# Performance work log

Measured on AMD Instinct MI355X. Metric: run time of the kernel, lower is better.

The kernel has to match this reference:

```python
import jax, jax.numpy as jnp
import numpy as np

B, N, MODES, WIDTH = 4, 8192, 12, 32
TWO = 2 * MODES  # 24
M_TOT = TWO * (TWO - 1)  # 552


def setup_inputs() -> dict:
    key = jax.random.key(0)
    ks = jax.random.split(key, 12)
    scale = 1.0 / (WIDTH * WIDTH)
    x = jax.random.uniform(ks[0], (B, N, 2), jnp.float32)
    fc0_w = jax.random.normal(ks[1], (2, WIDTH), jnp.float32) * 0.1
    fc0_b = jax.random.normal(ks[2], (WIDTH,), jnp.float32) * 0.05
    # 4 layers x {weights1, weights2}, stored as real/imag pairs (torch.rand cfloat ~ U[0,1)+1j*U[0,1))
    spec_w = jax.random.uniform(ks[3], (4, 2, WIDTH, WIDTH, MODES, MODES, 2), jnp.float32) * scale
    conv_w = jax.random.normal(ks[4], (4, WIDTH, WIDTH), jnp.float32) * 0.1  # Conv1d k=1 -> [O,I]
    conv_b = jax.random.normal(ks[5], (4, WIDTH), jnp.float32) * 0.05
    fc1_w = jax.random.normal(ks[6], (WIDTH, 128), jnp.float32) * 0.1
    fc1_b = jax.random.normal(ks[7], (128,), jnp.float32) * 0.05
    fc2_w = jax.random.normal(ks[8], (128, 1), jnp.float32) * 0.1
    fc2_b = jax.random.normal(ks[9], (1,), jnp.float32) * 0.05
    return {"x": x, "fc0_w": fc0_w, "fc0_b": fc0_b, "spec_w": spec_w,
            "conv_w": conv_w, "conv_b": conv_b, "fc1_w": fc1_w, "fc1_b": fc1_b,
            "fc2_w": fc2_w, "fc2_b": fc2_b}


def _vft_matrices(xp, yp):
    # xp, yp: [B, N], already min-shifted and scaled to [0, 6.28]
    kx = jnp.concatenate([jnp.arange(MODES), jnp.arange(-MODES, 0)]).astype(jnp.float32)       # [24]
    ky = jnp.concatenate([jnp.arange(MODES), jnp.arange(-(MODES - 1), 0)]).astype(jnp.float32)  # [23]
    Xm = kx[None, :, None] * xp[:, None, :]  # [B,24,N]
    Ym = ky[None, :, None] * yp[:, None, :]  # [B,23,N]
    # torch: X repeat(1,23,1) tiles blocks; Y repeat(1,1,24).reshape interleaves -> row j*24+i = X[i]+Y[j]
    phase = jnp.tile(Xm, (1, TWO - 1, 1)) + jnp.repeat(Ym, TWO, axis=1)  # [B,552,N]
    V_fwd = jnp.exp(-1j * phase)                    # [B,552,N] complex64
    V_inv = jnp.conj(V_fwd).transpose(0, 2, 1)      # [B,N,552]
    return V_fwd, V_inv


def _spectral_conv(h, V_fwd, V_inv, w1, w2):
    # h: [B,C,N] real; w1,w2: [C,C,M,M] complex
    b, c, n = h.shape
    # forward Vandermonde transform: bmm(V_fwd, h^T) then permute -> [B,C,552]
    x_ft = jnp.einsum('bmn,bnc->bcm', V_fwd, h.astype(jnp.complex64).transpose(0, 2, 1))
    x_ft = x_ft.reshape(b, c, TWO, TWO - 1)
    top = jnp.einsum('bixy,ioxy->boxy', x_ft[:, :, :MODES, :MODES], w1)
    bot = jnp.einsum('bixy,ioxy->boxy', x_ft[:, :, -MODES:, :MODES], w2)
    out_ft = jnp.zeros((b, WIDTH, TWO, MODES), jnp.complex64)
    out_ft = out_ft.at[:, :, :MODES, :MODES].set(top)
    out_ft = out_ft.at[:, :, -MODES:, :MODES].set(bot)
    x_ft = out_ft.reshape(b, WIDTH, 2 * MODES * MODES)  # [B,C,288]
    # conjugate-symmetric completion (flip over last two dims, as in source)
    x_ft2 = jnp.conj(jnp.flip(x_ft[..., TWO:], axis=(-2, -1)))  # [B,C,264]
    x_ft = jnp.concatenate([x_ft, x_ft2], axis=-1)  # [B,C,552]
    out = jnp.einsum('bnm,bmc->bcn', V_inv, x_ft.transpose(0, 2, 1))  # [B,C,N]
    return (out / n * 2).real


def reference(x, fc0_w, fc0_b, spec_w, conv_w, conv_b, fc1_w, fc1_b, fc2_w, fc2_b):
    gelu = lambda t: jax.nn.gelu(t, approximate=False)
    # VFT mutates x in-place by subtracting global mins (view semantics in torch)
    xp = x[:, :, 0] - jnp.min(x[:, :, 0])
    yp = x[:, :, 1] - jnp.min(x[:, :, 1])
    x_in = jnp.stack([xp, yp], axis=-1)  # what fc0 actually sees
    V_fwd, V_inv = _vft_matrices(xp * 6.28 / jnp.max(xp), yp * 6.28 / jnp.max(yp))
    h = (x_in @ fc0_w + fc0_b).transpose(0, 2, 1)  # [B,C,N]
    for l in range(4):
        w1 = spec_w[l, 0, ..., 0] + 1j * spec_w[l, 0, ..., 1]
        w2 = spec_w[l, 1, ..., 0] + 1j * spec_w[l, 1, ..., 1]
        x1 = _spectral_conv(h, V_fwd, V_inv, w1, w2)
        x2 = jnp.einsum('bin,oi->bon', h, conv_w[l]) + conv_b[l][None, :, None]
        h = x1 + x2
        if l < 3:
            h = gelu(h)
    h = h.transpose(0, 2, 1)  # [B,N,C]
    h = gelu(h @ fc1_w + fc1_b)
    return h @ fc2_w + fc2_b  # [B,N,1]
```

## Files before the change

### kernel.cpp

```cpp
#include <hip/hip_runtime.h>
#include <cmath>

#define NB 4
#define NN 8192
#define CH 32

typedef short short8 __attribute__((ext_vector_type(8)));
typedef float floatx4 __attribute__((ext_vector_type(4)));
typedef unsigned short ushort_t;

__device__ __forceinline__ unsigned short f2b(float f){
  unsigned u = __float_as_uint(f);
  u = u + 0x7FFFu + ((u >> 16) & 1u);
  return (unsigned short)(u >> 16);
}
__device__ __forceinline__ float b2f(unsigned short h){
  return __uint_as_float(((unsigned)h) << 16);
}
__device__ __forceinline__ float gelu_f(float v){
  return 0.5f * v * (1.0f + erff(v * 0.70710678118654752440f));
}
__device__ __forceinline__ int repk(int t){
  int j = t / 24, i = t - j * 24;
  if(j == 0)  return (i <= 12) ? i : -1;
  if(j <= 11) return 13 + (j - 1) * 24 + i;
  return (i == 12) ? 277 + (j - 12) : -1;
}
__device__ __forceinline__ int partner(int t){
  int j = t / 24, i = t - j * 24;
  return ((23 - j) % 23) * 24 + ((24 - i) % 24);
}
__device__ __forceinline__ int repT(int k){
  if(k < 13) return k;
  if(k < 277){ int m = k - 13; return (m / 24 + 1) * 24 + (m % 24); }
  return (k - 277 + 12) * 24 + 12;
}

__global__ __launch_bounds__(256) void k_pre(const float* __restrict__ spec,
    float2* __restrict__ wt, const float* __restrict__ x, float4* __restrict__ pmm,
    const float* __restrict__ fc1w, ushort_t* __restrict__ WB,
    const float* __restrict__ convw, ushort_t* __restrict__ WA)
{
  const int tid = threadIdx.x;
  if(blockIdx.x < 128){
    int g = blockIdx.x * 256 + tid;
    float a = x[(size_t)g * 2], b = x[(size_t)g * 2 + 1];
    float mn0 = a, mx0 = a, mn1 = b, mx1 = b;
    for(int off = 32; off > 0; off >>= 1){
      mn0 = fminf(mn0, __shfl_down(mn0, off));
      mx0 = fmaxf(mx0, __shfl_down(mx0, off));
      mn1 = fminf(mn1, __shfl_down(mn1, off));
      mx1 = fmaxf(mx1, __shfl_down(mx1, off));
    }
    __shared__ float4 wp[4];
    if((tid & 63) == 0) wp[tid >> 6] = make_float4(mn0, mn1, mx0, mx1);
    __syncthreads();
    if(tid == 0){
      float4 r = wp[0];
      for(int i2 = 1; i2 < 4; ++i2){
        float4 v = wp[i2];
        r.x = fminf(r.x, v.x); r.y = fminf(r.y, v.y);
        r.z = fmaxf(r.z, v.z); r.w = fmaxf(r.w, v.w);
      }
      pmm[blockIdx.x] = r;
    }
  } else if(blockIdx.x < 4736){
    int g = (blockIdx.x - 128) * 256 + tid;
    int o  = g & 31;
    int i  = (g >> 5) & 31;
    int rest = g >> 10;
    int pq = rest % 144;
    int ls = rest / 144;
    wt[g] = ((const float2*)spec)[(((size_t)(ls * 32 + i) * 32 + o) * 144 + pq)];
  } else {
    for(int s = tid; s < 512; s += 256){
      int jt = s >> 6, l = s & 63;
      int c = l & 15, qq = l >> 4;
      #pragma unroll
      for(int e = 0; e < 8; ++e){
        float wv = fc1w[(qq * 8 + e) * 128 + jt * 16 + c];
        ushort_t hi = f2b(wv);
        WB[(jt * 64 + l) * 8 + e] = hi;
        WB[4096 + (jt * 64 + l) * 8 + e] = f2b(wv - b2f(hi));
      }
    }
    for(int s = tid; s < 8192; s += 256){
      int l2   = s >> 11;
      int rem  = s & 2047;
      int limb = rem >> 10;
      int rem2 = rem & 1023;
      int half = rem2 >> 9;
      int le   = rem2 & 511;
      int lane = le >> 3, e = le & 7;
      int c = half * 16 + (lane & 15);
      int i = (lane >> 4) * 8 + e;
      float wv = convw[((size_t)l2 * 32 + c) * 32 + i] * 4096.0f;
      ushort_t hi = f2b(wv);
      WA[s] = limb ? f2b(wv - b2f(hi)) : hi;
    }
  }
}

__global__ __launch_bounds__(256) void k_vbuild(const float* __restrict__ x,
    const float4* __restrict__ pmm, const float* __restrict__ fw,
    const float* __restrict__ fb, ushort_t* __restrict__ AF, ushort_t* __restrict__ VTF,
    ushort_t* __restrict__ hbB, ushort_t* __restrict__ hbChi, ushort_t* __restrict__ hbClo)
{
  __shared__ ushort_t lds1[32 * 584];
  __shared__ float4 mmv;
  const int tid = threadIdx.x;
  if(tid < 64){
    float4 a = pmm[tid], c = pmm[tid + 64];
    float mn0 = fminf(a.x, c.x), mn1 = fminf(a.y, c.y);
    float mx0 = fmaxf(a.z, c.z), mx1 = fmaxf(a.w, c.w);
    for(int off = 32; off > 0; off >>= 1){
      mn0 = fminf(mn0, __shfl_down(mn0, off));
      mn1 = fminf(mn1, __shfl_down(mn1, off));
      mx0 = fmaxf(mx0, __shfl_down(mx0, off));
      mx1 = fmaxf(mx1, __shfl_down(mx1, off));
    }
    if(tid == 0) mmv = make_float4(mn0, mn1, mx0, mx1);
  }
  __syncthreads();
  const int nl = tid & 31, part = tid >> 5;
  const int b = blockIdx.x >> 8;
  const int nblk = blockIdx.x & 255;
  const int n = nblk * 32 + nl;
  float mn0 = mmv.x, mn1 = mmv.y, mx0 = mmv.z, mx1 = mmv.w;
  float x0 = x[(size_t)(b * NN + n) * 2]     - mn0;
  float x1 = x[(size_t)(b * NN + n) * 2 + 1] - mn1;
  float sp = x0 * (6.28f / (mx0 - mn0));
  float sq = x1 * (6.28f / (mx1 - mn1));
  float cx, sx, cy, sy;
  sincosf(sp, &sx, &cx);
  sincosf(sq, &sy, &cy);
  int j0 = part * 3;
  int j1 = (j0 + 3 < 23) ? j0 + 3 : 23;
  float ky0 = (j0 < 12) ? (float)j0 : (float)(j0 - 23);
  float cb, sb;
  sincosf(ky0 * sq, &sb, &cb);
  for(int j = j0; j < j1; ++j){
    float ca = 1.0f, sa = 0.0f;
    #pragma unroll
    for(int i = 0; i < 24; ++i){
      float vr = ca * cb - sa * sb;
      float vi = -(sa * cb + ca * sb);
      int t = j * 24 + i;
      int k = repk(t);
      if(k >= 0){
        lds1[nl * 584 + k]       = f2b(vr);
        lds1[nl * 584 + 288 + k] = f2b(vi);
      }
      float cn = ca * cx - sa * sx;
      float sn = sa * cx + ca * sx;
      if(i == 11) sn = -sn;
      ca = cn; sa = sn;
    }
    float cbn = cb * cy - sb * sy;
    float sbn = sb * cy + cb * sy;
    cb = cbn; sb = sbn;
  }
  __syncthreads();
  #pragma unroll
  for(int r = 0; r < 9; ++r){
    int c = tid + 256 * r;
    int t16 = c / 1152;
    int c2 = c - t16 * 1152;
    int kk = c2 >> 6;
    int rem = c2 & 63;
    int q = rem >> 4, n15 = rem & 15;
    short8 v = *(const short8*)(lds1 + (t16 * 16 + n15) * 584 + kk * 32 + q * 8);
    *(short8*)(VTF + ((size_t)((b * 512 + nblk * 2 + t16) * 18 + kk)) * 512
               + (q * 16 + n15) * 8) = v;
  }
  #pragma unroll
  for(int r = 0; r < 9; ++r){
    int c = tid + 256 * r;
    int st = c >> 6;
    int rem = c & 63;
    int q = rem >> 4, srow = rem & 15;
    int sg = st * 16 + srow;
    int s = (sg < 288) ? sg : sg - 288;
    int sinh_ = (sg >= 288);
    int p2 = s / 12, qq = s - p2 * 12;
    int t = p2 * 23 + qq;
    int k = repk(t);
    unsigned short flip = 0;
    if(k < 0){ k = repk(partner(t)); if(sinh_) flip = 0x8000; }
    int col = sinh_ ? 288 + k : k;
    ushort_t tmp[8];
    #pragma unroll
    for(int e = 0; e < 8; ++e)
      tmp[e] = lds1[(q * 8 + e) * 584 + col] ^ flip;
    *(short8*)(AF + ((size_t)((b * 36 + st) * 256 + nblk)) * 512
               + (q * 16 + srow) * 8) = *(short8*)tmp;
  }
  #pragma unroll
  for(int rr = 0; rr < 4; ++rr){
    int c2 = part + rr * 8;
    float v = fb[c2] + x0 * fw[c2] + x1 * fw[32 + c2];
    ushort_t hi = f2b(v), lo = f2b(v - b2f(hi));
    int half = c2 >> 4, cl = c2 & 15;
    hbB[(((size_t)(b * 2 + half) * 256 + nblk) * 512) + ((nl >> 3) * 16 + cl) * 8 + (nl & 7)] = hi;
    size_t ca = ((size_t)(b * 512 + nblk * 2 + (nl >> 4))) * 512
              + ((c2 >> 3) * 16 + (nl & 15)) * 8 + (c2 & 7);
    hbChi[ca] = hi; hbClo[ca] = lo;
  }
}

__global__ __launch_bounds__(256) void k_fwd(const ushort_t* __restrict__ AF,
    const ushort_t* __restrict__ hbB, float* __restrict__ xp)
{
  const int stp = blockIdx.x;
  const int ks = blockIdx.y;
  const int b  = blockIdx.z;
  const int w = threadIdx.x >> 6;
  const int lane = threadIdx.x & 63;
  const int row = lane & 15;
  const int q = lane >> 4;
  const int st0 = stp * 2;
  const size_t abase0 = ((size_t)(b * 36 + st0) * 256) * 512 + (q * 16 + row) * 8;
  const size_t abase1 = abase0 + (size_t)256 * 512;
  const size_t hB0 = ((size_t)(b * 2 + 0) * 256) * 512 + (size_t)lane * 8;
  const size_t hB1 = ((size_t)(b * 2 + 1) * 256) * 512 + (size_t)lane * 8;
  floatx4 aA0 = {0.f,0.f,0.f,0.f}, aA1 = {0.f,0.f,0.f,0.f};
  floatx4 aB0 = {0.f,0.f,0.f,0.f}, aB1 = {0.f,0.f,0.f,0.f};
  #pragma unroll
  for(int kk = 0; kk < 4; ++kk){
    int g = ks * 16 + w * 4 + kk;
    short8 A0 = *(const short8*)(AF + abase0 + (size_t)g * 512);
    short8 A1 = *(const short8*)(AF + abase1 + (size_t)g * 512);
    short8 B0 = *(const short8*)(hbB + hB0 + (size_t)g * 512);
    short8 B1 = *(const short8*)(hbB + hB1 + (size_t)g * 512);
    aA0 = __builtin_amdgcn_mfma_f32_16x16x32_bf16(A0, B0, aA0, 0, 0, 0);
    aA1 = __builtin_amdgcn_mfma_f32_16x16x32_bf16(A0, B1, aA1, 0, 0, 0);
    aB0 = __builtin_amdgcn_mfma_f32_16x16x32_bf16(A1, B0, aB0, 0, 0, 0);
    aB1 = __builtin_amdgcn_mfma_f32_16x16x32_bf16(A1, B1, aB1, 0, 0, 0);
  }
  __shared__ float red[4 * 512];
  const int e = threadIdx.x;
  const int eo = e & 31;
  #pragma unroll
  for(int r = 0; r < 4; ++r){
    int rrow = q * 4 + r;
    red[w * 512 + rrow * 32 + row]      = aA0[r];
    red[w * 512 + rrow * 32 + 16 + row] = aA1[r];
  }
  __syncthreads();
  {
    float v0 = red[e] + red[512 + e] + red[1024 + e] + red[1536 + e];
    float v1 = red[e + 256] + red[512 + e + 256] + red[1024 + e + 256] + red[1536 + e + 256];
    size_t r0 = (size_t)(b * 576 + st0 * 16 + (e >> 5));
    xp[(r0 * 16 + ks) * 32 + eo]       = v0;
    xp[((r0 + 8) * 16 + ks) * 32 + eo] = v1;
  }
  __syncthreads();
  #pragma unroll
  for(int r = 0; r < 4; ++r){
    int rrow = q * 4 + r;
    red[w * 512 + rrow * 32 + row]      = aB0[r];
    red[w * 512 + rrow * 32 + 16 + row] = aB1[r];
  }
  __syncthreads();
  {
    float v0 = red[e] + red[512 + e] + red[1024 + e] + red[1536 + e];
    float v1 = red[e + 256] + red[512 + e + 256] + red[1024 + e + 256] + red[1536 + e + 256];
    size_t r0 = (size_t)(b * 576 + (st0 + 1) * 16 + (e >> 5));
    xp[(r0 * 16 + ks) * 32 + eo]       = v0;
    xp[((r0 + 8) * 16 + ks) * 32 + eo] = v1;
  }
}

__global__ __launch_bounds__(256) void k_mixg(const float* __restrict__ xp,
    const float2* __restrict__ wt, ushort_t* __restrict__ ghi, ushort_t* __restrict__ glof,
    int layer)
{
  const int wv = threadIdx.x >> 6;
  const int lane = threadIdx.x & 63;
  const int k = blockIdx.x;
  const int b = blockIdx.y;
  const int t = repT(k);
  const int j = t / 24, i = t - j * 24;
  const int u = partner(t);
  const bool unpaired = (i == 12) || (u == t);
  const int idxT = (t < 288) ? t : 575 - t;  const bool cfT = (t >= 288);
  const int idxU = (u < 288) ? u : 575 - u;  const bool cfU = (u >= 288);
  __shared__ float Xs[2][64];
  __shared__ float FrP[2][2][32], FiP[2][2][32];
  {
    const int m = wv & 1, hf = wv >> 1;
    int idx = m ? idxU : idxT;
    int rrow = hf ? 288 + idx : idx;
    const float* sb = xp + (size_t)(b * 576 + rrow) * 512;
    float4 a = *(const float4*)(sb + lane * 4);
    float4 c = *(const float4*)(sb + 256 + lane * 4);
    a.x += c.x; a.y += c.y; a.z += c.z; a.w += c.w;
    #pragma unroll
    for(int mk = 8; mk <= 32; mk <<= 1){
      a.x += __shfl_xor(a.x, mk);
      a.y += __shfl_xor(a.y, mk);
      a.z += __shfl_xor(a.z, mk);
      a.w += __shfl_xor(a.w, mk);
    }
    if(lane < 8){
      int o0 = hf * 32 + lane * 4;
      Xs[m][o0 + 0] = a.x;
      Xs[m][o0 + 1] = a.y;
      Xs[m][o0 + 2] = a.z;
      Xs[m][o0 + 3] = a.w;
    }
  }
  __syncthreads();
  {
    const int m = wv & 1, ih = wv >> 1;
    int idx = m ? idxU : idxT;
    int p2 = idx / 12, qq = idx - p2 * 12;
    int sel = (p2 < 12) ? 0 : 1;
    int pq = (p2 % 12) * 12 + qq;
    const float2* wb = wt + ((size_t)((layer * 2 + sel) * 144 + pq)) * 1024;
    if(lane < 32){
      const int o = lane;
      float fr = 0.f, fi = 0.f;
      #pragma unroll
      for(int ii = 0; ii < 16; ++ii){
        int i2 = ih * 16 + ii;
        float xr = Xs[m][i2], xi = Xs[m][32 + i2];
        float2 wvv = wb[i2 * 32 + o];
        fr += xr * wvv.x - xi * wvv.y;
        fi += xr * wvv.y + xi * wvv.x;
      }
      FrP[m][ih][o] = fr; FiP[m][ih][o] = fi;
    }
  }
  __syncthreads();
  if(wv == 0 && lane < 32){
    const int c = lane;
    const int srcT = cfT ? 31 - c : c;
    const int srcU = cfU ? 31 - c : c;
    float fax = FrP[0][0][srcT] + FrP[0][1][srcT];
    float fay = FiP[0][0][srcT] + FiP[0][1][srcT];
    float fbx = FrP[1][0][srcU] + FrP[1][1][srcU];
    float fby = FiP[1][0][srcU] + FiP[1][1][srcU];
    float gr = fax;
    float gi = cfT ? -fay : fay;
    if(!unpaired){
      gr += fbx;
      gi -= (cfU ? -fby : fby);
    }
    unsigned short hr = f2b(gr); float lr = gr - b2f(hr);
    unsigned short hi2 = f2b(gi); float li = gi - b2f(hi2);
    size_t base = (size_t)(b * CH + c) * 576;
    ghi[base + k] = hr;          ghi[base + 288 + k] = hi2;
    int hhc = c >> 4, cl = c & 15;
    int kk1 = k >> 5, q1 = (k >> 3) & 3, e1 = k & 7;
    size_t fb2 = (size_t)(b * 2 + hhc) * 18;
    glof[(fb2 + kk1) * 512 + (q1 * 16 + cl) * 8 + e1]     = f2b(lr);
    glof[(fb2 + 9 + kk1) * 512 + (q1 * 16 + cl) * 8 + e1] = f2b(li);
  }
}

template<int LAST>
__global__ __launch_bounds__(512, 6) void k_inv(const ushort_t* __restrict__ VTF,
    const ushort_t* __restrict__ ghi, const ushort_t* __restrict__ glof,
    const float* __restrict__ cbias, int layer,
    const ushort_t* __restrict__ hbCi_hi, const ushort_t* __restrict__ hbCi_lo,
    ushort_t* __restrict__ hbBo, ushort_t* __restrict__ hbCo_hi,
    ushort_t* __restrict__ hbCo_lo,
    const float* __restrict__ b1, const float* __restrict__ w2,
    const float* __restrict__ b2, float* __restrict__ out,
    const ushort_t* __restrict__ WBg, const ushort_t* __restrict__ WA)
{
  __shared__ ushort_t GH[32][584];
  const int tid = threadIdx.x;
  const int b = blockIdx.y;
  const int bx = blockIdx.x;
  for(int idx = tid; idx < 2304; idx += 512){
    int ch = idx / 72, g8 = (idx - ch * 72) * 8;
    if(g8 < 576)
      *(short8*)&GH[ch][g8] = *(const short8*)(ghi + (size_t)(b * CH + ch) * 576 + g8);
  }
  __syncthreads();
  const int lane = tid & 63;
  const int w = tid >> 6;
  const int tl = w >> 1;
  const int hh = w & 1;
  const int row = lane & 15, q = lane >> 4;
  const int t16 = bx * 4 + tl;
  const ushort_t* vb = VTF + ((size_t)(b * 512 + t16) * 18) * 512 + lane * 8;
  const ushort_t* gl = glof + ((size_t)(b * 2 + hh) * 18) * 512 + lane * 8;
  const int gr = hh * 16 + row, ko = q * 8;
  floatx4 ah = {0.f,0.f,0.f,0.f}, al = {0.f,0.f,0.f,0.f};
  #pragma unroll
  for(int kk = 0; kk < 18; ++kk){
    short8 Bv = *(const short8*)(vb + (size_t)kk * 512);
    short8 Ah = *(const short8*)&GH[gr][ko + kk * 32];
    short8 Al = *(const short8*)(gl + (size_t)kk * 512);
    ah = __builtin_amdgcn_mfma_f32_16x16x32_bf16(Ah, Bv, ah, 0, 0, 0);
    al = __builtin_amdgcn_mfma_f32_16x16x32_bf16(Al, Bv, al, 0, 0, 0);
  }
  {
    short8 Whi = *(const short8*)(WA + ((size_t)((layer * 2 + 0) * 2 + hh)) * 512 + lane * 8);
    short8 Wlo = *(const short8*)(WA + ((size_t)((layer * 2 + 1) * 2 + hh)) * 512 + lane * 8);
    short8 Bhi = *(const short8*)(hbCi_hi + ((size_t)(b * 512 + t16)) * 512 + lane * 8);
    short8 Blo = *(const short8*)(hbCi_lo + ((size_t)(b * 512 + t16)) * 512 + lane * 8);
    ah = __builtin_amdgcn_mfma_f32_16x16x32_bf16(Whi, Bhi, ah, 0, 0, 0);
    al = __builtin_amdgcn_mfma_f32_16x16x32_bf16(Wlo, Bhi, al, 0, 0, 0);
    ah = __builtin_amdgcn_mfma_f32_16x16x32_bf16(Whi, Blo, ah, 0, 0, 0);
  }
  floatx4 accF = ah + al;
  const float sc = 2.0f / 8192.0f;
  float cb[4];
  #pragma unroll
  for(int r = 0; r < 4; ++r) cb[r] = cbias[layer * 32 + hh * 16 + q * 4 + r];
  if constexpr(!LAST){
    const int n = bx * 64 + tl * 16 + row;
    const int g = n >> 5, qb = (n >> 3) & 3, e2 = n & 7;
    #pragma unroll
    for(int r = 0; r < 4; ++r){
      int c = hh * 16 + q * 4 + r;
      float v = gelu_f(accF[r] * sc + cb[r]);
      ushort_t hi = f2b(v), lo = f2b(v - b2f(hi));
      hbBo[(((size_t)(b * 2 + hh) * 256 + g) * 512) + (qb * 16 + (q * 4 + r)) * 8 + e2] = hi;
      size_t ca = ((size_t)(b * 512 + t16)) * 512 + ((c >> 3) * 16 + row) * 8 + (c & 7);
      hbCo_hi[ca] = hi; hbCo_lo[ca] = lo;
    }
  } else {
    __shared__ ushort_t hHi[64][36];
    __shared__ ushort_t hLo[64][36];
    __shared__ float part[2][64];
    {
      ushort_t H[4], L[4];
      #pragma unroll
      for(int r = 0; r < 4; ++r){
        float v = accF[r] * sc + cb[r];
        H[r] = f2b(v); L[r] = f2b(v - b2f(H[r]));
      }
      uint2 uu;
      uu.x = (unsigned)H[0] | ((unsigned)H[1] << 16);
      uu.y = (unsigned)H[2] | ((unsigned)H[3] << 16);
      *(uint2*)&hHi[tl * 16 + row][hh * 16 + q * 4] = uu;
      uu.x = (unsigned)L[0] | ((unsigned)L[1] << 16);
      uu.y = (unsigned)L[2] | ((unsigned)L[3] << 16);
      *(uint2*)&hLo[tl * 16 + row][hh * 16 + q * 4] = uu;
    }
    __syncthreads();
    const int cl = row;
    short8 Ahi = *(const short8*)&hHi[tl * 16 + cl][q * 8];
    short8 Alo = *(const short8*)&hLo[tl * 16 + cl][q * 8];
    float S0 = 0.f, S1 = 0.f, S2 = 0.f, S3 = 0.f;
    #pragma unroll
    for(int jt2 = 0; jt2 < 4; ++jt2){
      int jt = hh * 4 + jt2;
      short8 Bhi = *(const short8*)(WBg + (jt * 64 + lane) * 8);
      short8 Blo = *(const short8*)(WBg + 4096 + (jt * 64 + lane) * 8);
      floatx4 acc = {0.f, 0.f, 0.f, 0.f};
      acc = __builtin_amdgcn_mfma_f32_16x16x32_bf16(Ahi, Bhi, acc, 0, 0, 0);
      acc = __builtin_amdgcn_mfma_f32_16x16x32_bf16(Alo, Bhi, acc, 0, 0, 0);
      acc = __builtin_amdgcn_mfma_f32_16x16x32_bf16(Ahi, Blo, acc, 0, 0, 0);
      float bv = b1[jt * 16 + cl], wv = w2[jt * 16 + cl];
      S0 = fmaf(gelu_f(acc[0] + bv), wv, S0);
      S1 = fmaf(gelu_f(acc[1] + bv), wv, S1);
      S2 = fmaf(gelu_f(acc[2] + bv), wv, S2);
      S3 = fmaf(gelu_f(acc[3] + bv), wv, S3);
    }
    #pragma unroll
    for(int off = 8; off; off >>= 1){
      S0 += __shfl_xor(S0, off, 16);
      S1 += __shfl_xor(S1, off, 16);
      S2 += __shfl_xor(S2, off, 16);
      S3 += __shfl_xor(S3, off, 16);
    }
    if(cl == 0){
      int pb = tl * 16 + q * 4;
      part[hh][pb + 0] = S0;
      part[hh][pb + 1] = S1;
      part[hh][pb + 2] = S2;
      part[hh][pb + 3] = S3;
    }
    __syncthreads();
    if(tid < 64)
      out[(size_t)b * NN + bx * 64 + tid] = part[0][tid] + part[1][tid] + b2[0];
  }
}

extern "C" void kernel_launch(void* const* d_in, const int* in_sizes, int n_in,
                              void* d_out, int out_size, void* d_ws, size_t ws_size,
                              hipStream_t stream)
{
  const float* x      = (const float*)d_in[0];
  const float* fc0_w  = (const float*)d_in[1];
  const float* fc0_b  = (const float*)d_in[2];
  const float* spec_w = (const float*)d_in[3];
  const float* conv_w = (const float*)d_in[4];
  const float* conv_b = (const float*)d_in[5];
  const float* fc1_w  = (const float*)d_in[6];
  const float* fc1_b  = (const float*)d_in[7];
  const float* fc2_w  = (const float*)d_in[8];
  const float* fc2_b  = (const float*)d_in[9];
  float* out = (float*)d_out;

  char* w = (char*)d_ws;
  const size_t OFF_PMM  = 0;
  const size_t OFF_WT   = 4096;
  const size_t OFF_AF   = OFF_WT  + 9437184;
  const size_t OFF_VTF  = OFF_AF  + 37748736;
  const size_t OFF_HB0  = OFF_VTF + 37748736;
  const size_t OFF_HB1  = OFF_HB0 + 2097152;
  const size_t OFF_HC0  = OFF_HB1 + 2097152;
  const size_t OFF_HC1  = OFF_HC0 + 2097152;
  const size_t OFF_HL0  = OFF_HC1 + 2097152;
  const size_t OFF_HL1  = OFF_HL0 + 2097152;
  const size_t OFF_XP   = OFF_HL1 + 2097152;
  const size_t OFF_GHI  = OFF_XP  + 4718592;
  const size_t OFF_GLO  = OFF_GHI + 147456;
  const size_t OFF_WB   = OFF_GLO + 147456;
  const size_t OFF_WA   = OFF_WB  + 16384;

  float4* pmm    = (float4*)(w + OFF_PMM);
  float2* wt     = (float2*)(w + OFF_WT);
  ushort_t* AF   = (ushort_t*)(w + OFF_AF);
  ushort_t* VTF  = (ushort_t*)(w + OFF_VTF);
  ushort_t* hbB[2]  = { (ushort_t*)(w + OFF_HB0), (ushort_t*)(w + OFF_HB1) };
  ushort_t* hbChi[2] = { (ushort_t*)(w + OFF_HC0), (ushort_t*)(w + OFF_HC1) };
  ushort_t* hbClo[2] = { (ushort_t*)(w + OFF_HL0), (ushort_t*)(w + OFF_HL1) };
  float* xp      = (float*)(w + OFF_XP);
  ushort_t* ghi  = (ushort_t*)(w + OFF_GHI);
  ushort_t* glof = (ushort_t*)(w + OFF_GLO);
  ushort_t* WB   = (ushort_t*)(w + OFF_WB);
  ushort_t* WA   = (ushort_t*)(w + OFF_WA);

  hipLaunchKernelGGL(k_pre, dim3(4737), dim3(256), 0, stream, spec_w, wt, x, pmm,
                     fc1_w, WB, conv_w, WA);
  hipLaunchKernelGGL(k_vbuild, dim3(1024), dim3(256), 0, stream, x, pmm,
                     fc0_w, fc0_b, AF, VTF, hbB[0], hbChi[0], hbClo[0]);

  for(int l = 0; l < 4; ++l){
    int in = l & 1, outb = 1 - in;
    hipLaunchKernelGGL(k_fwd, dim3(18, 16, NB), dim3(256), 0, stream, AF, hbB[in], xp);
    hipLaunchKernelGGL(k_mixg, dim3(288, NB), dim3(256), 0, stream, xp, wt, ghi, glof, l);
    if(l < 3)
      hipLaunchKernelGGL(k_inv<0>, dim3(128, NB), dim3(512), 0, stream, VTF, ghi, glof,
                         conv_b, l, hbChi[in], hbClo[in],
                         hbB[outb], hbChi[outb], hbClo[outb],
                         fc1_b, fc2_w, fc2_b, out, WB, WA);
    else
      hipLaunchKernelGGL(k_inv<1>, dim3(128, NB), dim3(512), 0, stream, VTF, ghi, glof,
                         conv_b, l, hbChi[in], hbClo[in],
                         hbB[outb], hbChi[outb], hbClo[outb],
                         fc1_b, fc2_w, fc2_b, out, WB, WA);
  }
  (void)in_sizes; (void)n_in; (void)out_size; (void)ws_size;
}
```

Baseline: 224.2 us.

## Store spectral hi coefficients in MFMA fragment layout and shrink k_inv blocks

k_mixg now writes the bf16 high part of the mixed spectral coefficients directly in MFMA fragment order, the same layout already used for the low part. k_inv then loads these A-fragments straight from global memory instead of staging the whole 32x576 coefficient matrix into LDS behind a block barrier. With no large LDS buffer left, k_inv uses 256-thread blocks covering 32 points each, doubling the grid. The goal is to remove the per-block LDS staging and sync and to raise occupancy. In exchange, every wave re-reads the coefficient fragments from global or L2, twice as many blocks do this, and the hbBo stores become narrower.

```diff
diff --git a/kernel.cpp b/kernel.cpp
--- a/kernel.cpp
+++ b/kernel.cpp
@@ -272,7 +272,7 @@
 }
 
 __global__ __launch_bounds__(256) void k_mixg(const float* __restrict__ xp,
-    const float2* __restrict__ wt, ushort_t* __restrict__ ghi, ushort_t* __restrict__ glof,
+    const float2* __restrict__ wt, ushort_t* __restrict__ ghif, ushort_t* __restrict__ glof,
     int layer)
 {
   const int wv = threadIdx.x >> 6;
@@ -349,19 +349,20 @@
     }
     unsigned short hr = f2b(gr); float lr = gr - b2f(hr);
     unsigned short hi2 = f2b(gi); float li = gi - b2f(hi2);
-    size_t base = (size_t)(b * CH + c) * 576;
-    ghi[base + k] = hr;          ghi[base + 288 + k] = hi2;
     int hhc = c >> 4, cl = c & 15;
     int kk1 = k >> 5, q1 = (k >> 3) & 3, e1 = k & 7;
     size_t fb2 = (size_t)(b * 2 + hhc) * 18;
-    glof[(fb2 + kk1) * 512 + (q1 * 16 + cl) * 8 + e1]     = f2b(lr);
-    glof[(fb2 + 9 + kk1) * 512 + (q1 * 16 + cl) * 8 + e1] = f2b(li);
+    size_t off = (size_t)(q1 * 16 + cl) * 8 + e1;
+    ghif[(fb2 + kk1) * 512 + off]     = hr;
+    ghif[(fb2 + 9 + kk1) * 512 + off] = hi2;
+    glof[(fb2 + kk1) * 512 + off]     = f2b(lr);
+    glof[(fb2 + 9 + kk1) * 512 + off] = f2b(li);
   }
 }
 
 template<int LAST>
-__global__ __launch_bounds__(512, 6) void k_inv(const ushort_t* __restrict__ VTF,
-    const ushort_t* __restrict__ ghi, const ushort_t* __restrict__ glof,
+__global__ __launch_bounds__(256, 6) void k_inv(const ushort_t* __restrict__ VTF,
+    const ushort_t* __restrict__ ghif, const ushort_t* __restrict__ glof,
     const float* __restrict__ cbias, int layer,
     const ushort_t* __restrict__ hbCi_hi, const ushort_t* __restrict__ hbCi_lo,
     ushort_t* __restrict__ hbBo, ushort_t* __restrict__ hbCo_hi,
@@ -370,30 +371,23 @@
     const float* __restrict__ b2, float* __restrict__ out,
     const ushort_t* __restrict__ WBg, const ushort_t* __restrict__ WA)
 {
-  __shared__ ushort_t GH[32][584];
   const int tid = threadIdx.x;
   const int b = blockIdx.y;
   const int bx = blockIdx.x;
-  for(int idx = tid; idx < 2304; idx += 512){
-    int ch = idx / 72, g8 = (idx - ch * 72) * 8;
-    if(g8 < 576)
-      *(short8*)&GH[ch][g8] = *(const short8*)(ghi + (size_t)(b * CH + ch) * 576 + g8);
-  }
-  __syncthreads();
   const int lane = tid & 63;
   const int w = tid >> 6;
   const int tl = w >> 1;
   const int hh = w & 1;
   const int row = lane & 15, q = lane >> 4;
-  const int t16 = bx * 4 + tl;
+  const int t16 = bx * 2 + tl;
   const ushort_t* vb = VTF + ((size_t)(b * 512 + t16) * 18) * 512 + lane * 8;
+  const ushort_t* gh = ghif + ((size_t)(b * 2 + hh) * 18) * 512 + lane * 8;
   const ushort_t* gl = glof + ((size_t)(b * 2 + hh) * 18) * 512 + lane * 8;
-  const int gr = hh * 16 + row, ko = q * 8;
   floatx4 ah = {0.f,0.f,0.f,0.f}, al = {0.f,0.f,0.f,0.f};
   #pragma unroll
   for(int kk = 0; kk < 18; ++kk){
     short8 Bv = *(const short8*)(vb + (size_t)kk * 512);
-    short8 Ah = *(const short8*)&GH[gr][ko + kk * 32];
+    short8 Ah = *(const short8*)(gh + (size_t)kk * 512);
     short8 Al = *(const short8*)(gl + (size_t)kk * 512);
     ah = __builtin_amdgcn_mfma_f32_16x16x32_bf16(Ah, Bv, ah, 0, 0, 0);
     al = __builtin_amdgcn_mfma_f32_16x16x32_bf16(Al, Bv, al, 0, 0, 0);
@@ -413,21 +407,21 @@
   #pragma unroll
   for(int r = 0; r < 4; ++r) cb[r] = cbias[layer * 32 + hh * 16 + q * 4 + r];
   if constexpr(!LAST){
-    const int n = bx * 64 + tl * 16 + row;
-    const int g = n >> 5, qb = (n >> 3) & 3, e2 = n & 7;
+    const int n = bx * 32 + tl * 16 + row;
+    const int g2 = n >> 5, qb = (n >> 3) & 3, e2 = n & 7;
     #pragma unroll
     for(int r = 0; r < 4; ++r){
       int c = hh * 16 + q * 4 + r;
       float v = gelu_f(accF[r] * sc + cb[r]);
       ushort_t hi = f2b(v), lo = f2b(v - b2f(hi));
-      hbBo[(((size_t)(b * 2 + hh) * 256 + g) * 512) + (qb * 16 + (q * 4 + r)) * 8 + e2] = hi;
+      hbBo[(((size_t)(b * 2 + hh) * 256 + g2) * 512) + (qb * 16 + (q * 4 + r)) * 8 + e2] = hi;
       size_t ca = ((size_t)(b * 512 + t16)) * 512 + ((c >> 3) * 16 + row) * 8 + (c & 7);
       hbCo_hi[ca] = hi; hbCo_lo[ca] = lo;
     }
   } else {
-    __shared__ ushort_t hHi[64][36];
-    __shared__ ushort_t hLo[64][36];
-    __shared__ float part[2][64];
+    __shared__ ushort_t hHi[32][36];
+    __shared__ ushort_t hLo[32][36];
+    __shared__ float part[2][32];
     {
       ushort_t H[4], L[4];
       #pragma unroll
@@ -478,8 +472,8 @@
       part[hh][pb + 3] = S3;
     }
     __syncthreads();
-    if(tid < 64)
-      out[(size_t)b * NN + bx * 64 + tid] = part[0][tid] + part[1][tid] + b2[0];
+    if(tid < 32)
+      out[(size_t)b * NN + bx * 32 + tid] = part[0][tid] + part[1][tid] + b2[0];
   }
 }
 
@@ -511,8 +505,8 @@
   const size_t OFF_HL0  = OFF_HC1 + 2097152;
   const size_t OFF_HL1  = OFF_HL0 + 2097152;
   const size_t OFF_XP   = OFF_HL1 + 2097152;
-  const size_t OFF_GHI  = OFF_XP  + 4718592;
-  const size_t OFF_GLO  = OFF_GHI + 147456;
+  const size_t OFF_GHF  = OFF_XP  + 4718592;
+  const size_t OFF_GLO  = OFF_GHF + 147456;
   const size_t OFF_WB   = OFF_GLO + 147456;
   const size_t OFF_WA   = OFF_WB  + 16384;
 
@@ -524,7 +518,7 @@
   ushort_t* hbChi[2] = { (ushort_t*)(w + OFF_HC0), (ushort_t*)(w + OFF_HC1) };
   ushort_t* hbClo[2] = { (ushort_t*)(w + OFF_HL0), (ushort_t*)(w + OFF_HL1) };
   float* xp      = (float*)(w + OFF_XP);
-  ushort_t* ghi  = (ushort_t*)(w + OFF_GHI);
+  ushort_t* ghif = (ushort_t*)(w + OFF_GHF);
   ushort_t* glof = (ushort_t*)(w + OFF_GLO);
   ushort_t* WB   = (ushort_t*)(w + OFF_WB);
   ushort_t* WA   = (ushort_t*)(w + OFF_WA);
@@ -537,14 +531,14 @@
   for(int l = 0; l < 4; ++l){
     int in = l & 1, outb = 1 - in;
     hipLaunchKernelGGL(k_fwd, dim3(18, 16, NB), dim3(256), 0, stream, AF, hbB[in], xp);
-    hipLaunchKernelGGL(k_mixg, dim3(288, NB), dim3(256), 0, stream, xp, wt, ghi, glof, l);
+    hipLaunchKernelGGL(k_mixg, dim3(288, NB), dim3(256), 0, stream, xp, wt, ghif, glof, l);
     if(l < 3)
-      hipLaunchKernelGGL(k_inv<0>, dim3(128, NB), dim3(512), 0, stream, VTF, ghi, glof,
+      hipLaunchKernelGGL(k_inv<0>, dim3(256, NB), dim3(256), 0, stream, VTF, ghif, glof,
                          conv_b, l, hbChi[in], hbClo[in],
                          hbB[outb], hbChi[outb], hbClo[outb],
                          fc1_b, fc2_w, fc2_b, out, WB, WA);
     else
-      hipLaunchKernelGGL(k_inv<1>, dim3(128, NB), dim3(512), 0, stream, VTF, ghi, glof,
+      hipLaunchKernelGGL(k_inv<1>, dim3(256, NB), dim3(256), 0, stream, VTF, ghif, glof,
                          conv_b, l, hbChi[in], hbClo[in],
                          hbB[outb], hbChi[outb], hbClo[outb],
                          fc1_b, fc2_w, fc2_b, out, WB, WA);
```

Result: no change. 224.5 us (+0.1%).
